# Kernel optimization log

Hardware: AMD Instinct MI355X
Metric: run time of the kernel (lower is better)

## Reference

```python
import jax, jax.numpy as jnp
import numpy as np


def _kernel_features(data, proj, is_query):
    # data: [B,S,H,D], proj: [R,D] -> features [B,S,H,R]  (FAVOR+ positive softmax kernel)
    d = data.shape[-1]
    r = proj.shape[0]
    data_normalizer = 1.0 / jnp.sqrt(jnp.sqrt(jnp.float32(d)))
    ratio = 1.0 / jnp.sqrt(jnp.float32(r))
    data_hat = jnp.einsum('bshd,rd->bshr', data_normalizer * data, proj)
    diag = (jnp.sum(data * data, axis=-1) * 0.5) * (data_normalizer * data_normalizer)
    diag = diag[..., None]  # [B,S,H,1]
    if is_query:
        m = jnp.max(data_hat, axis=-1, keepdims=True)
    else:
        m = jnp.max(data_hat)
    return ratio * (jnp.exp(data_hat - diag - m) + 1e-4)


def reference(query, key, value, Wq, bq, Wk, bk, Wv, bv, Wo, bo, proj):
    proj = jax.lax.stop_gradient(proj)
    # QKV projections: [B,S,Dm] -> [B,S,H,Dh]
    q = jnp.einsum('bsd,dhk->bshk', query, Wq) + bq
    k = jnp.einsum('bsd,dhk->bshk', key, Wk) + bk
    v = jnp.einsum('bsd,dhv->bshv', value, Wv) + bv
    q_hat = _kernel_features(q, proj, True)   # [B,S,H,R]
    k_hat = _kernel_features(k, proj, False)  # [B,S,H,R]
    # kv aggregation: 'aecr,aecd->acrd'
    kv = jnp.einsum('bshr,bshv->bhrv', k_hat, v)          # [B,H,R,Dv]
    out = jnp.einsum('bshr,bhrv->bshv', q_hat, kv)        # [B,S,H,Dv]
    # normalization: k1 = sum_s k_hat ('abcd,abc->acd'), denom = q_hat . k1
    k1 = jnp.sum(k_hat, axis=1)                           # [B,H,R]
    denom = jnp.einsum('bshr,bhr->bsh', q_hat, k1)        # [B,S,H]
    out = out / denom[..., None]
    # output projection: combine heads
    return jnp.einsum('bshv,hvd->bsd', out, Wo) + bo


def setup_inputs() -> dict:
    key0 = jax.random.key(0)
    ks = jax.random.split(key0, 10)
    B, S, Dm, H, Dh, R = 4, 4096, 1024, 16, 64, 256
    scale = 1.0 / np.sqrt(Dm)
    # Gaussian orthogonal random matrix [R, Dh], scaling=0 (chi row norms)
    blk = jax.random.normal(ks[8], (R, Dh))
    qmat, _ = jnp.linalg.qr(blk)  # R >= Dh -> q is [R, Dh]
    mult = jnp.linalg.norm(jax.random.normal(ks[9], (R, Dh)), axis=1)
    proj = mult[:, None] * qmat
    return {
        'query': jax.random.normal(ks[0], (B, S, Dm)),
        'key': jax.random.normal(ks[1], (B, S, Dm)),
        'value': jax.random.normal(ks[2], (B, S, Dm)),
        'Wq': jax.random.normal(ks[3], (Dm, H, Dh)) * scale,
        'bq': jnp.zeros((H, Dh)),
        'Wk': jax.random.normal(ks[4], (Dm, H, Dh)) * scale,
        'bk': jnp.zeros((H, Dh)),
        'Wv': jax.random.normal(ks[5], (Dm, H, Dh)) * scale,
        'bv': jnp.zeros((H, Dh)),
        'Wo': jax.random.normal(ks[6], (H, Dh, Dm)) * scale,
        'bo': jnp.zeros((Dm,)),
        'proj': proj,
    }
```

## Files before the change

kernel.cpp:

```cpp
#include <hip/hip_runtime.h>

typedef unsigned short u16;
typedef unsigned int u32;
typedef __attribute__((ext_vector_type(4))) float f32x4;
typedef __attribute__((ext_vector_type(8))) short bf16x8;

#define B_ 4
#define S_ 4096
#define H_ 16
#define DH_ 64
#define R_ 256
#define DM_ 1024
#define M_ 16384
#define ROWSTR 1024

__device__ __forceinline__ float bf2f(u16 u) {
  union { u32 i; float f; } v; v.i = ((u32)u) << 16; return v.f;
}
__device__ __forceinline__ u16 f2bf(float f) {
  union { float f; u32 i; } v; v.f = f;
  u32 x = v.i;
  return (u16)((x + 0x7FFFu + ((x >> 16) & 1u)) >> 16);
}
__device__ __forceinline__ void lds_load16(const void* g, void* l) {
  __builtin_amdgcn_global_load_lds((__attribute__((address_space(1))) void*)(g),
                                   (__attribute__((address_space(3))) void*)(l), 16, 0, 0);
}
__device__ __forceinline__ int vt_idx(int dv, int s) {
  return dv * 64 + (s ^ (dv & 0x38));
}

__global__ __launch_bounds__(256) void dtype_probe_k(const u16* __restrict__ q,
                                                     int* __restrict__ flag) {
  __shared__ int cnt_s;
  int tid = threadIdx.x;
  if (tid == 0) cnt_s = 0;
  __syncthreads();
  int c = 0;
  for (int i = tid; i < 1024; i += 256) {
    u32 e = ((u32)q[i] >> 7) & 0xFF;
    c += (e >= 134) ? 1 : 0;
  }
  atomicAdd(&cnt_s, c);
  __syncthreads();
  if (tid == 0) flag[0] = (cnt_s > 32) ? 1 : 0;
}

template <int WLO>
__global__ __launch_bounds__(256) void split_k(const void* __restrict__ src,
                                               u16* __restrict__ hi, u16* __restrict__ lo,
                                               const int* __restrict__ flag) {
  const bool f32m = flag[0] != 0;
  size_t i = ((size_t)blockIdx.x * 256 + threadIdx.x) * 8;
  if (f32m) {
    f32x4 a = *(const f32x4*)((const float*)src + i);
    f32x4 b = *(const f32x4*)((const float*)src + i + 4);
    bf16x8 h, l;
    for (int e = 0; e < 4; ++e) {
      u16 ha = f2bf(a[e]); h[e] = (short)ha; l[e] = (short)f2bf(a[e] - bf2f(ha));
      u16 hb = f2bf(b[e]); h[4 + e] = (short)hb; l[4 + e] = (short)f2bf(b[e] - bf2f(hb));
    }
    *(bf16x8*)(hi + i) = h;
    if (WLO) *(bf16x8*)(lo + i) = l;
  } else {
    bf16x8 h = *(const bf16x8*)((const u16*)src + i);
    *(bf16x8*)(hi + i) = h;
    if (WLO) {
      bf16x8 z = {0, 0, 0, 0, 0, 0, 0, 0};
      *(bf16x8*)(lo + i) = z;
    }
  }
}

__global__ __launch_bounds__(256) void transpose4_k(
    const void* __restrict__ s0, const void* __restrict__ s1,
    const void* __restrict__ s2, const void* __restrict__ s3,
    u16* __restrict__ dh0, u16* __restrict__ dl0, u16* __restrict__ dh1, u16* __restrict__ dl1,
    u16* __restrict__ dh2, u16* __restrict__ dl2, u16* __restrict__ dh3, u16* __restrict__ dl3,
    const int* __restrict__ flag) {
  __shared__ float tile[32][33];
  const bool f32m = flag[0] != 0;
  int z = blockIdx.z;
  const void* src = (z == 0) ? s0 : (z == 1) ? s1 : (z == 2) ? s2 : s3;
  u16* dh = (z == 0) ? dh0 : (z == 1) ? dh1 : (z == 2) ? dh2 : dh3;
  u16* dl = (z == 0) ? dl0 : (z == 1) ? dl1 : (z == 2) ? dl2 : dl3;
  int tx = threadIdx.x, ty = threadIdx.y;
  int x0 = blockIdx.x * 32, y0 = blockIdx.y * 32;
  for (int i = ty; i < 32; i += 8) {
    size_t idx = (size_t)(y0 + i) * DM_ + x0 + tx;
    tile[i][tx] = f32m ? ((const float*)src)[idx] : bf2f(((const u16*)src)[idx]);
  }
  __syncthreads();
  for (int i = ty; i < 32; i += 8) {
    float t = tile[tx][i];
    u16 hi = f2bf(t);
    size_t o = (size_t)(x0 + i) * DM_ + y0 + tx;
    dh[o] = hi;
    dl[o] = f2bf(t - bf2f(hi));
  }
}

__global__ __launch_bounds__(256) void projcvt_k(const void* __restrict__ p,
                                                 u16* __restrict__ ph, u16* __restrict__ pl,
                                                 const int* __restrict__ flag) {
  const bool f32m = flag[0] != 0;
  int i = blockIdx.x * 256 + threadIdx.x;
  if (i < R_ * DH_) {
    float t = f32m ? ((const float*)p)[i] : bf2f(((const u16*)p)[i]);
    u16 hi = f2bf(t);
    ph[i] = hi;
    pl[i] = f2bf(t - bf2f(hi));
  }
}

template <int PREC, int OUTMODE>
__global__ __launch_bounds__(256) void gemm_k(
    const u16* __restrict__ Ah, const u16* __restrict__ Al,
    const u16* __restrict__ Bth, const u16* __restrict__ Btl,
    const void* __restrict__ bias, void* __restrict__ C, u16* __restrict__ Clo,
    const int* __restrict__ flag) {
  __shared__ __attribute__((aligned(16))) u16 Ash[128 * 32];
  __shared__ __attribute__((aligned(16))) u16 Bsh[128 * 32];
  __shared__ __attribute__((aligned(16))) u16 Asl[128 * 32];
  __shared__ __attribute__((aligned(16))) u16 Bsl[128 * 32];
  const bool f32m = flag[0] != 0;
  const int K = DM_, N = DM_;
  const int tid = threadIdx.x, wave = tid >> 6, lane = tid & 63;
  const int lr = lane & 15, qd = lane >> 4;
  const int bm = blockIdx.x, bn = blockIdx.y;
  const int m0 = (wave & 1) * 64, n0 = (wave >> 1) * 64;
  const u16* Abh = Ah + (size_t)bm * 128 * K;
  const u16* Bbh = Bth + (size_t)bn * 128 * K;
  const u16* Abl = (PREC == 3) ? Al + (size_t)bm * 128 * K : nullptr;
  const u16* Bbl = (PREC == 3) ? Btl + (size_t)bn * 128 * K : nullptr;
  f32x4 zero = {0.f, 0.f, 0.f, 0.f};
  f32x4 acc[4][4];
  for (int i = 0; i < 4; ++i) for (int j = 0; j < 4; ++j) acc[i][j] = zero;
  for (int k0 = 0; k0 < K; k0 += 32) {
    __syncthreads();
    for (int t = 0; t < 2; ++t) {
      int c = wave + t * 4;
      int row = c * 16 + (lane >> 2);
      int kc = (lane & 3) * 8;
      size_t go = (size_t)row * K + k0 + kc;
      lds_load16(Abh + go, (void*)&Ash[c * 512]);
      lds_load16(Bbh + go, (void*)&Bsh[c * 512]);
      if (PREC == 3) {
        lds_load16(Abl + go, (void*)&Asl[c * 512]);
        lds_load16(Bbl + go, (void*)&Bsl[c * 512]);
      }
    }
    __syncthreads();
    bf16x8 ah[4], bh[4];
    for (int i = 0; i < 4; ++i) ah[i] = *(const bf16x8*)&Ash[(m0 + i * 16 + lr) * 32 + qd * 8];
    for (int j = 0; j < 4; ++j) bh[j] = *(const bf16x8*)&Bsh[(n0 + j * 16 + lr) * 32 + qd * 8];
    for (int i = 0; i < 4; ++i)
      for (int j = 0; j < 4; ++j)
        acc[i][j] = __builtin_amdgcn_mfma_f32_16x16x32_bf16(ah[i], bh[j], acc[i][j], 0, 0, 0);
    if (PREC == 3) {
      bf16x8 al[4], bl[4];
      for (int i = 0; i < 4; ++i) al[i] = *(const bf16x8*)&Asl[(m0 + i * 16 + lr) * 32 + qd * 8];
      for (int j = 0; j < 4; ++j) bl[j] = *(const bf16x8*)&Bsl[(n0 + j * 16 + lr) * 32 + qd * 8];
      for (int i = 0; i < 4; ++i)
        for (int j = 0; j < 4; ++j) {
          acc[i][j] = __builtin_amdgcn_mfma_f32_16x16x32_bf16(ah[i], bl[j], acc[i][j], 0, 0, 0);
          acc[i][j] = __builtin_amdgcn_mfma_f32_16x16x32_bf16(al[i], bh[j], acc[i][j], 0, 0, 0);
        }
    }
  }
  for (int j = 0; j < 4; ++j) {
    int n = bn * 128 + n0 + j * 16 + lr;
    float bv = f32m ? ((const float*)bias)[n] : bf2f(((const u16*)bias)[n]);
    for (int i = 0; i < 4; ++i) {
      int mr = bm * 128 + m0 + i * 16 + qd * 4;
      for (int r2 = 0; r2 < 4; ++r2) {
        float x = acc[i][j][r2] + bv;
        size_t o = (size_t)(mr + r2) * N + n;
        if (OUTMODE == 0) {
          ((u16*)C)[o] = f2bf(x);
        } else if (OUTMODE == 1) {
          u16 hi = f2bf(x);
          ((u16*)C)[o] = hi;
          Clo[o] = f2bf(x - bf2f(hi));
        } else {
          if (f32m) ((float*)C)[o] = x;
          else ((u16*)C)[o] = f2bf(x);
        }
      }
    }
  }
}

__global__ __launch_bounds__(256) void feat_max_k(
    const u16* __restrict__ khi, const u16* __restrict__ klo,
    const u16* __restrict__ ph, const u16* __restrict__ pl, float* __restrict__ pm) {
  __shared__ __attribute__((aligned(16))) u16 kth[64 * 64];
  __shared__ __attribute__((aligned(16))) u16 ktl[64 * 64];
  __shared__ float red[4];
  const int tid = threadIdx.x, wave = tid >> 6, lane = tid & 63;
  const int lr = lane & 15, qd = lane >> 4;
  int bid = blockIdx.x;
  int chunk = bid & 63, bh = bid >> 6;
  int b = bh >> 4, h = bh & 15;
  size_t base = (((size_t)b * S_ + (size_t)chunk * 64) * H_ + h) * DH_;
  {
    int s = tid >> 2, dg = (tid & 3) * 16;
    size_t go = base + (size_t)s * ROWSTR + dg;
    *(bf16x8*)&kth[s * 64 + dg]     = *(const bf16x8*)(khi + go);
    *(bf16x8*)&kth[s * 64 + dg + 8] = *(const bf16x8*)(khi + go + 8);
    *(bf16x8*)&ktl[s * 64 + dg]     = *(const bf16x8*)(klo + go);
    *(bf16x8*)&ktl[s * 64 + dg + 8] = *(const bf16x8*)(klo + go + 8);
  }
  __syncthreads();
  const int r0 = wave * 64;
  f32x4 zero = {0.f, 0.f, 0.f, 0.f};
  f32x4 acc[4][4];
  for (int i = 0; i < 4; ++i) for (int j = 0; j < 4; ++j) acc[i][j] = zero;
  for (int ks = 0; ks < 2; ++ks) {
    bf16x8 ah[4], al[4], bh_[4], bl_[4];
    for (int i = 0; i < 4; ++i) {
      ah[i] = *(const bf16x8*)&kth[(i * 16 + lr) * 64 + ks * 32 + qd * 8];
      al[i] = *(const bf16x8*)&ktl[(i * 16 + lr) * 64 + ks * 32 + qd * 8];
    }
    for (int j = 0; j < 4; ++j) {
      size_t o = (size_t)(r0 + j * 16 + lr) * DH_ + ks * 32 + qd * 8;
      bh_[j] = *(const bf16x8*)(ph + o);
      bl_[j] = *(const bf16x8*)(pl + o);
    }
    for (int i = 0; i < 4; ++i)
      for (int j = 0; j < 4; ++j) {
        acc[i][j] = __builtin_amdgcn_mfma_f32_16x16x32_bf16(ah[i], bh_[j], acc[i][j], 0, 0, 0);
        acc[i][j] = __builtin_amdgcn_mfma_f32_16x16x32_bf16(al[i], bh_[j], acc[i][j], 0, 0, 0);
        acc[i][j] = __builtin_amdgcn_mfma_f32_16x16x32_bf16(ah[i], bl_[j], acc[i][j], 0, 0, 0);
      }
  }
  float mx = -3.0e38f;
  for (int i = 0; i < 4; ++i) for (int j = 0; j < 4; ++j) for (int r2 = 0; r2 < 4; ++r2)
    mx = fmaxf(mx, acc[i][j][r2]);
  for (int m2 = 1; m2 < 64; m2 <<= 1) mx = fmaxf(mx, __shfl_xor(mx, m2, 64));
  if (lane == 0) red[wave] = mx;
  __syncthreads();
  if (tid == 0)
    pm[bid] = 0.3535533905932738f * fmaxf(fmaxf(red[0], red[1]), fmaxf(red[2], red[3]));
}

__global__ __launch_bounds__(256) void reduce_max_k(const float* __restrict__ pm,
                                                    float* __restrict__ mout) {
  __shared__ float buf[256];
  int t = threadIdx.x;
  float m = -3.0e38f;
  for (int i = t; i < 4096; i += 256) m = fmaxf(m, pm[i]);
  buf[t] = m;
  __syncthreads();
  if (t < 64) {
    float v = fmaxf(fmaxf(buf[t], buf[t + 64]), fmaxf(buf[t + 128], buf[t + 192]));
    for (int m2 = 1; m2 < 64; m2 <<= 1) v = fmaxf(v, __shfl_xor(v, m2, 64));
    if (t == 0) mout[0] = v;
  }
}

__global__ __launch_bounds__(256) void kv_accum_k(
    const u16* __restrict__ khi, const u16* __restrict__ klo,
    const u16* __restrict__ vv,
    const u16* __restrict__ ph, const u16* __restrict__ pl,
    const float* __restrict__ mptr,
    float* __restrict__ pkv, float* __restrict__ pk1, int ipb) {
  __shared__ __attribute__((aligned(16))) u16 kth[64 * 64];
  __shared__ __attribute__((aligned(16))) u16 ktl[64 * 64];
  __shared__ __attribute__((aligned(16))) u16 vTh[64 * 64];
  __shared__ __attribute__((aligned(16))) u16 khatT[256 * 72];
  __shared__ float dpart[4][64];
  __shared__ float diagl[64];
  const int tid = threadIdx.x, wave = tid >> 6, lane = tid & 63;
  const int lr = lane & 15, qd = lane >> 4;
  int bid = blockIdx.x;
  int bh = bid & 63, c = bid >> 6;
  int b = bh >> 4, h = bh & 15;
  const float mglob = mptr[0];
  const float nrm = 0.3535533905932738f;
  const float ratio = 0.0625f;
  size_t base0 = (((size_t)b * S_ + (size_t)c * ipb * 64) * H_ + h) * DH_;
  f32x4 zero = {0.f, 0.f, 0.f, 0.f};
  f32x4 acc[4][4];
  for (int i = 0; i < 4; ++i) for (int j = 0; j < 4; ++j) acc[i][j] = zero;
  float k1p[4][4];
  for (int i = 0; i < 4; ++i) for (int r2 = 0; r2 < 4; ++r2) k1p[i][r2] = 0.f;
  const int r0 = wave * 64;
  bf16x8 pfa_h[2][4], pfa_l[2][4];
  for (int ks = 0; ks < 2; ++ks)
    for (int i = 0; i < 4; ++i) {
      size_t o = (size_t)(r0 + i * 16 + lr) * DH_ + ks * 32 + qd * 8;
      pfa_h[ks][i] = *(const bf16x8*)(ph + o);
      pfa_l[ks][i] = *(const bf16x8*)(pl + o);
    }
  for (int it = 0; it < ipb; ++it) {
    size_t ibase = base0 + (size_t)it * 64 * ROWSTR;
    __syncthreads();
    {
      int s = tid >> 2, dg = (tid & 3) * 16;
      size_t go = ibase + (size_t)s * ROWSTR + dg;
      *(bf16x8*)&kth[s * 64 + dg]     = *(const bf16x8*)(khi + go);
      *(bf16x8*)&kth[s * 64 + dg + 8] = *(const bf16x8*)(khi + go + 8);
      *(bf16x8*)&ktl[s * 64 + dg]     = *(const bf16x8*)(klo + go);
      *(bf16x8*)&ktl[s * 64 + dg + 8] = *(const bf16x8*)(klo + go + 8);
    }
    {
      int s = tid >> 2;
      int dv0 = (tid & 3) * 16;
      size_t go = ibase + (size_t)s * ROWSTR + dv0;
      bf16x8 h0 = *(const bf16x8*)(vv + go);
      bf16x8 h1 = *(const bf16x8*)(vv + go + 8);
      for (int e = 0; e < 8; ++e) {
        vTh[vt_idx(dv0 + e, s)] = (u16)h0[e];
        vTh[vt_idx(dv0 + 8 + e, s)] = (u16)h1[e];
      }
    }
    __syncthreads();
    {
      int s = tid & 63, qr = tid >> 6;
      bf16x8 h0 = *(const bf16x8*)&kth[s * 64 + qr * 16];
      bf16x8 h1 = *(const bf16x8*)&kth[s * 64 + qr * 16 + 8];
      bf16x8 l0 = *(const bf16x8*)&ktl[s * 64 + qr * 16];
      bf16x8 l1 = *(const bf16x8*)&ktl[s * 64 + qr * 16 + 8];
      float sum = 0.f;
      for (int e = 0; e < 8; ++e) { float f = bf2f((u16)h0[e]) + bf2f((u16)l0[e]); sum += f * f; }
      for (int e = 0; e < 8; ++e) { float f = bf2f((u16)h1[e]) + bf2f((u16)l1[e]); sum += f * f; }
      dpart[qr][s] = sum;
    }
    __syncthreads();
    if (tid < 64)
      diagl[tid] = 0.0625f * (dpart[0][tid] + dpart[1][tid] + dpart[2][tid] + dpart[3][tid]);
    f32x4 a1[4][4];
    for (int i = 0; i < 4; ++i) for (int j = 0; j < 4; ++j) a1[i][j] = zero;
    for (int ks = 0; ks < 2; ++ks) {
      bf16x8 bh_[4], bl_[4];
      for (int j = 0; j < 4; ++j) {
        bh_[j] = *(const bf16x8*)&kth[(j * 16 + lr) * 64 + ks * 32 + qd * 8];
        bl_[j] = *(const bf16x8*)&ktl[(j * 16 + lr) * 64 + ks * 32 + qd * 8];
      }
      for (int i = 0; i < 4; ++i)
        for (int j = 0; j < 4; ++j) {
          a1[i][j] = __builtin_amdgcn_mfma_f32_16x16x32_bf16(pfa_h[ks][i], bh_[j], a1[i][j], 0, 0, 0);
          a1[i][j] = __builtin_amdgcn_mfma_f32_16x16x32_bf16(pfa_l[ks][i], bh_[j], a1[i][j], 0, 0, 0);
          a1[i][j] = __builtin_amdgcn_mfma_f32_16x16x32_bf16(pfa_h[ks][i], bl_[j], a1[i][j], 0, 0, 0);
        }
    }
    __syncthreads();
    for (int i = 0; i < 4; ++i)
      for (int r2 = 0; r2 < 4; ++r2) {
        int r = r0 + i * 16 + qd * 4 + r2;
        for (int j = 0; j < 4; ++j) {
          int s = j * 16 + lr;
          float arg = fminf(nrm * a1[i][j][r2] - diagl[s] - mglob, 30.f);
          float kh = ratio * (__expf(arg) + 1e-4f);
          u16 khb = f2bf(kh);
          khatT[r * 72 + s] = khb;
          k1p[i][r2] += bf2f(khb);
        }
      }
    __syncthreads();
    for (int ks = 0; ks < 2; ++ks) {
      bf16x8 af[4], bh_[4];
      for (int i = 0; i < 4; ++i)
        af[i] = *(const bf16x8*)&khatT[(r0 + i * 16 + lr) * 72 + ks * 32 + qd * 8];
      for (int j = 0; j < 4; ++j) {
        int dv = j * 16 + lr;
        bh_[j] = *(const bf16x8*)&vTh[vt_idx(dv, ks * 32 + qd * 8)];
      }
      for (int i = 0; i < 4; ++i)
        for (int j = 0; j < 4; ++j)
          acc[i][j] = __builtin_amdgcn_mfma_f32_16x16x32_bf16(af[i], bh_[j], acc[i][j], 0, 0, 0);
    }
  }
  size_t obase = ((size_t)c * 64 + bh) * R_;
  for (int i = 0; i < 4; ++i)
    for (int j = 0; j < 4; ++j)
      for (int r2 = 0; r2 < 4; ++r2) {
        int r = r0 + i * 16 + qd * 4 + r2;
        int dv = j * 16 + lr;
        pkv[(obase + r) * DH_ + dv] = acc[i][j][r2];
      }
  for (int i = 0; i < 4; ++i)
    for (int r2 = 0; r2 < 4; ++r2) {
      float v = k1p[i][r2];
      v += __shfl_xor(v, 1, 64); v += __shfl_xor(v, 2, 64);
      v += __shfl_xor(v, 4, 64); v += __shfl_xor(v, 8, 64);
      if (lr == 0) pk1[obase + r0 + i * 16 + qd * 4 + r2] = v;
    }
}

__global__ __launch_bounds__(256) void kv_reduce_k(
    const float* __restrict__ pkv, const float* __restrict__ pk1,
    u16* __restrict__ kvTh, u16* __restrict__ kvTl, float* __restrict__ k1, int nchunk) {
  __shared__ float tile[64][65];
  int bh = blockIdx.x, tl = blockIdx.y, t = threadIdx.x;
  if (tl == 0) {
    float s = 0.f;
    for (int c = 0; c < nchunk; ++c) s += pk1[((size_t)c * 64 + bh) * R_ + t];
    k1[(size_t)bh * R_ + t] = s;
  }
  for (int e = 0; e < 16; ++e) {
    int idx = e * 256 + t;
    int rl = idx >> 6, dv = idx & 63;
    float s = 0.f;
    for (int c = 0; c < nchunk; ++c)
      s += pkv[(((size_t)c * 64 + bh) * R_ + tl * 64 + rl) * DH_ + dv];
    tile[rl][dv] = s;
  }
  __syncthreads();
  for (int e = 0; e < 16; ++e) {
    int idx = e * 256 + t;
    int dv = idx >> 6, rl = idx & 63;
    float s = tile[rl][dv];
    u16 hi = f2bf(s);
    size_t o = ((size_t)bh * DH_ + dv) * R_ + tl * 64 + rl;
    kvTh[o] = hi;
    kvTl[o] = f2bf(s - bf2f(hi));
  }
}

__global__ __launch_bounds__(256) void q_out_k(
    const u16* __restrict__ qhi, const u16* __restrict__ qlo,
    const u16* __restrict__ ph, const u16* __restrict__ pl,
    const u16* __restrict__ kvTh, const u16* __restrict__ kvTl,
    const float* __restrict__ k1, u16* __restrict__ op) {
  __shared__ __attribute__((aligned(16))) u16 qth[64 * 64];
  __shared__ __attribute__((aligned(16))) u16 qtl[64 * 64];
  __shared__ __attribute__((aligned(16))) u16 qh[64 * 264];
  __shared__ float wrm[4][64];
  __shared__ float dpart[4][64];
  __shared__ float diagl[64];
  __shared__ float dinv[64];
  const int tid = threadIdx.x, wave = tid >> 6, lane = tid & 63;
  const int lr = lane & 15, qd = lane >> 4;
  int bid = blockIdx.x;
  int chunk = bid & 63, bh = bid >> 6;
  int b = bh >> 4, h = bh & 15;
  const float nrm = 0.3535533905932738f;
  const float ratio = 0.0625f;
  size_t base = (((size_t)b * S_ + (size_t)chunk * 64) * H_ + h) * DH_;
  const u16* kvThb = kvTh + (size_t)bh * DH_ * R_;
  const u16* kvTlb = kvTl + (size_t)bh * DH_ * R_;
  const float* k1b = k1 + (size_t)bh * R_;
  {
    int s = tid >> 2, dg = (tid & 3) * 16;
    size_t go = base + (size_t)s * ROWSTR + dg;
    *(bf16x8*)&qth[s * 64 + dg]     = *(const bf16x8*)(qhi + go);
    *(bf16x8*)&qth[s * 64 + dg + 8] = *(const bf16x8*)(qhi + go + 8);
    *(bf16x8*)&qtl[s * 64 + dg]     = *(const bf16x8*)(qlo + go);
    *(bf16x8*)&qtl[s * 64 + dg + 8] = *(const bf16x8*)(qlo + go + 8);
  }
  __syncthreads();
  {
    int s = tid & 63, qr = tid >> 6;
    bf16x8 h0 = *(const bf16x8*)&qth[s * 64 + qr * 16];
    bf16x8 h1 = *(const bf16x8*)&qth[s * 64 + qr * 16 + 8];
    bf16x8 l0 = *(const bf16x8*)&qtl[s * 64 + qr * 16];
    bf16x8 l1 = *(const bf16x8*)&qtl[s * 64 + qr * 16 + 8];
    float sum = 0.f;
    for (int e = 0; e < 8; ++e) { float f = bf2f((u16)h0[e]) + bf2f((u16)l0[e]); sum += f * f; }
    for (int e = 0; e < 8; ++e) { float f = bf2f((u16)h1[e]) + bf2f((u16)l1[e]); sum += f * f; }
    dpart[qr][s] = sum;
  }
  __syncthreads();
  if (tid < 64)
    diagl[tid] = 0.0625f * (dpart[0][tid] + dpart[1][tid] + dpart[2][tid] + dpart[3][tid]);
  f32x4 zero = {0.f, 0.f, 0.f, 0.f};
  f32x4 a1[4][4];
  for (int i = 0; i < 4; ++i) for (int j = 0; j < 4; ++j) a1[i][j] = zero;
  const int r0 = wave * 64;
  for (int ks = 0; ks < 2; ++ks) {
    bf16x8 ah[4], al[4], bh_[4], bl_[4];
    for (int i = 0; i < 4; ++i) {
      ah[i] = *(const bf16x8*)&qth[(i * 16 + lr) * 64 + ks * 32 + qd * 8];
      al[i] = *(const bf16x8*)&qtl[(i * 16 + lr) * 64 + ks * 32 + qd * 8];
    }
    for (int j = 0; j < 4; ++j) {
      size_t o = (size_t)(r0 + j * 16 + lr) * DH_ + ks * 32 + qd * 8;
      bh_[j] = *(const bf16x8*)(ph + o);
      bl_[j] = *(const bf16x8*)(pl + o);
    }
    for (int i = 0; i < 4; ++i)
      for (int j = 0; j < 4; ++j) {
        a1[i][j] = __builtin_amdgcn_mfma_f32_16x16x32_bf16(ah[i], bh_[j], a1[i][j], 0, 0, 0);
        a1[i][j] = __builtin_amdgcn_mfma_f32_16x16x32_bf16(al[i], bh_[j], a1[i][j], 0, 0, 0);
        a1[i][j] = __builtin_amdgcn_mfma_f32_16x16x32_bf16(ah[i], bl_[j], a1[i][j], 0, 0, 0);
      }
  }
  for (int i = 0; i < 4; ++i)
    for (int r2 = 0; r2 < 4; ++r2) {
      float v = fmaxf(fmaxf(a1[i][0][r2], a1[i][1][r2]), fmaxf(a1[i][2][r2], a1[i][3][r2]));
      v = fmaxf(v, __shfl_xor(v, 1, 64)); v = fmaxf(v, __shfl_xor(v, 2, 64));
      v = fmaxf(v, __shfl_xor(v, 4, 64)); v = fmaxf(v, __shfl_xor(v, 8, 64));
      if (lr == 0) wrm[wave][i * 16 + qd * 4 + r2] = v;
    }
  __syncthreads();
  for (int i = 0; i < 4; ++i)
    for (int r2 = 0; r2 < 4; ++r2) {
      int s = i * 16 + qd * 4 + r2;
      float rmax = fmaxf(fmaxf(wrm[0][s], wrm[1][s]), fmaxf(wrm[2][s], wrm[3][s]));
      float dg = diagl[s];
      for (int j = 0; j < 4; ++j) {
        float arg = fminf(nrm * (a1[i][j][r2] - rmax) - dg, 30.f);
        float qv = ratio * (__expf(arg) + 1e-4f);
        qh[s * 264 + r0 + j * 16 + lr] = f2bf(qv);
      }
    }
  __syncthreads();
  {
    float sum = 0.f;
    int s = lane;
    for (int rr = 0; rr < 8; ++rr) {
      bf16x8 v = *(const bf16x8*)&qh[s * 264 + wave * 64 + rr * 8];
      for (int e = 0; e < 8; ++e) sum += bf2f((u16)v[e]) * k1b[wave * 64 + rr * 8 + e];
    }
    dpart[wave][s] = sum;
  }
  __syncthreads();
  if (tid < 64) {
    float dn = dpart[0][tid] + dpart[1][tid] + dpart[2][tid] + dpart[3][tid];
    dinv[tid] = 1.0f / fmaxf(dn, 1e-35f);
  }
  __syncthreads();
  f32x4 a2[2][2];
  for (int i = 0; i < 2; ++i) for (int j = 0; j < 2; ++j) a2[i][j] = zero;
  const int sw = (wave & 1) * 32, dw = (wave >> 1) * 32;
  for (int ks = 0; ks < 8; ++ks) {
    bf16x8 af[2], bh_[2], bl_[2];
    for (int i = 0; i < 2; ++i)
      af[i] = *(const bf16x8*)&qh[(sw + i * 16 + lr) * 264 + ks * 32 + qd * 8];
    for (int j = 0; j < 2; ++j) {
      size_t o = (size_t)(dw + j * 16 + lr) * R_ + ks * 32 + qd * 8;
      bh_[j] = *(const bf16x8*)(kvThb + o);
      bl_[j] = *(const bf16x8*)(kvTlb + o);
    }
    for (int i = 0; i < 2; ++i)
      for (int j = 0; j < 2; ++j) {
        a2[i][j] = __builtin_amdgcn_mfma_f32_16x16x32_bf16(af[i], bh_[j], a2[i][j], 0, 0, 0);
        a2[i][j] = __builtin_amdgcn_mfma_f32_16x16x32_bf16(af[i], bl_[j], a2[i][j], 0, 0, 0);
      }
  }
  for (int i = 0; i < 2; ++i)
    for (int r2 = 0; r2 < 4; ++r2) {
      int s = sw + i * 16 + qd * 4 + r2;
      float di = dinv[s];
      for (int j = 0; j < 2; ++j) {
        int dv = dw + j * 16 + lr;
        op[base + (size_t)s * ROWSTR + dv] = f2bf(a2[i][j][r2] * di);
      }
    }
}

extern "C" void kernel_launch(void* const* d_in, const int* in_sizes, int n_in,
                              void* d_out, int out_size, void* d_ws, size_t ws_size,
                              hipStream_t stream) {
  const void* query = d_in[0];
  const void* key   = d_in[1];
  const void* value = d_in[2];
  const void* Wq = d_in[3];
  const void* bq = d_in[4];
  const void* Wk = d_in[5];
  const void* bk = d_in[6];
  const void* Wv = d_in[7];
  const void* bv = d_in[8];
  const void* Wo = d_in[9];
  const void* bo = d_in[10];
  const void* proj = d_in[11];

  char* w = (char*)d_ws;
  const size_t MB = 1024 * 1024;
  u16* WqT_h = (u16*)(w + 0 * MB);
  u16* WqT_l = (u16*)(w + 2 * MB);
  u16* WkT_h = (u16*)(w + 4 * MB);
  u16* WkT_l = (u16*)(w + 6 * MB);
  u16* WvT_h = (u16*)(w + 8 * MB);
  u16* WvT_l = (u16*)(w + 10 * MB);
  u16* WoT_h = (u16*)(w + 12 * MB);
  u16* WoT_l = (u16*)(w + 14 * MB);
  u16* kq_hi = (u16*)(w + 16 * MB);
  u16* kq_lo = (u16*)(w + 48 * MB);
  u16* vop   = (u16*)(w + 80 * MB);
  float* pk1 = (float*)(w + 112 * MB);
  u16* kvTh  = (u16*)(w + 112 * MB + 512 * 1024);
  u16* kvTl  = (u16*)(w + 114 * MB + 512 * 1024);
  float* k1  = (float*)(w + 116 * MB + 512 * 1024);
  float* pm  = (float*)(w + 116 * MB + 640 * 1024);
  float* mg  = (float*)(w + 116 * MB + 700 * 1024);
  u16* p_hi  = (u16*)(w + 116 * MB + 768 * 1024);
  u16* p_lo  = (u16*)(w + 116 * MB + 832 * 1024);
  int* flag  = (int*)(w + 116 * MB + 900 * 1024);
  float* pkv  = (float*)(w + 117 * MB);
  u16* inA_hi = (u16*)(w + 117 * MB);
  u16* inA_lo = (u16*)(w + 149 * MB);
  int nchunk = 4;
  int ipb = 64 / nchunk;

  dtype_probe_k<<<1, 256, 0, stream>>>((const u16*)query, flag);
  transpose4_k<<<dim3(32, 32, 4), dim3(32, 8), 0, stream>>>(
      Wq, Wk, Wv, Wo, WqT_h, WqT_l, WkT_h, WkT_l, WvT_h, WvT_l, WoT_h, WoT_l, flag);
  projcvt_k<<<64, 256, 0, stream>>>(proj, p_hi, p_lo, flag);
  split_k<1><<<8192, 256, 0, stream>>>(key, inA_hi, inA_lo, flag);
  gemm_k<3, 1><<<dim3(128, 8), 256, 0, stream>>>(inA_hi, inA_lo, WkT_h, WkT_l, bk, kq_hi, kq_lo, flag);
  split_k<0><<<8192, 256, 0, stream>>>(value, inA_hi, nullptr, flag);
  gemm_k<1, 0><<<dim3(128, 8), 256, 0, stream>>>(inA_hi, nullptr, WvT_h, nullptr, bv, vop, nullptr, flag);
  feat_max_k<<<4096, 256, 0, stream>>>(kq_hi, kq_lo, p_hi, p_lo, pm);
  reduce_max_k<<<1, 256, 0, stream>>>(pm, mg);
  kv_accum_k<<<nchunk * 64, 256, 0, stream>>>(kq_hi, kq_lo, vop, p_hi, p_lo, mg, pkv, pk1, ipb);
  kv_reduce_k<<<dim3(64, 4), 256, 0, stream>>>(pkv, pk1, kvTh, kvTl, k1, nchunk);
  split_k<1><<<8192, 256, 0, stream>>>(query, inA_hi, inA_lo, flag);
  gemm_k<3, 1><<<dim3(128, 8), 256, 0, stream>>>(inA_hi, inA_lo, WqT_h, WqT_l, bq, kq_hi, kq_lo, flag);
  q_out_k<<<4096, 256, 0, stream>>>(kq_hi, kq_lo, p_hi, p_lo, kvTh, kvTl, k1, vop);
  gemm_k<1, 2><<<dim3(128, 8), 256, 0, stream>>>(vop, nullptr, WoT_h, nullptr, bo, d_out, nullptr, flag);
}
```

Measured before the change: 916.0 us.

## Use direct-to-LDS swizzled loads, alias LDS buffers, fuse denom, raise chunking

Result: no change. 901.2 us (-1.6%).

```diff
diff --git a/kernel.cpp b/kernel.cpp
--- a/kernel.cpp
+++ b/kernel.cpp
@@ -203,24 +203,26 @@
   int chunk = bid & 63, bh = bid >> 6;
   int b = bh >> 4, h = bh & 15;
   size_t base = (((size_t)b * S_ + (size_t)chunk * 64) * H_ + h) * DH_;
-  {
-    int s = tid >> 2, dg = (tid & 3) * 16;
-    size_t go = base + (size_t)s * ROWSTR + dg;
-    *(bf16x8*)&kth[s * 64 + dg]     = *(const bf16x8*)(khi + go);
-    *(bf16x8*)&kth[s * 64 + dg + 8] = *(const bf16x8*)(khi + go + 8);
-    *(bf16x8*)&ktl[s * 64 + dg]     = *(const bf16x8*)(klo + go);
-    *(bf16x8*)&ktl[s * 64 + dg + 8] = *(const bf16x8*)(klo + go + 8);
+  for (int t = 0; t < 2; ++t) {
+    int cc = wave + t * 4;
+    int rr = cc * 8 + (lane >> 3);
+    int csw = (((lane & 7) ^ (rr & 7)) << 3);
+    size_t go = base + (size_t)rr * ROWSTR + csw;
+    lds_load16(khi + go, (void*)&kth[cc * 512]);
+    lds_load16(klo + go, (void*)&ktl[cc * 512]);
   }
   __syncthreads();
   const int r0 = wave * 64;
   f32x4 zero = {0.f, 0.f, 0.f, 0.f};
   f32x4 acc[4][4];
   for (int i = 0; i < 4; ++i) for (int j = 0; j < 4; ++j) acc[i][j] = zero;
+  __builtin_amdgcn_s_setprio(1);
   for (int ks = 0; ks < 2; ++ks) {
     bf16x8 ah[4], al[4], bh_[4], bl_[4];
     for (int i = 0; i < 4; ++i) {
-      ah[i] = *(const bf16x8*)&kth[(i * 16 + lr) * 64 + ks * 32 + qd * 8];
-      al[i] = *(const bf16x8*)&ktl[(i * 16 + lr) * 64 + ks * 32 + qd * 8];
+      int cof = (ks * 32 + qd * 8) ^ ((lr & 7) << 3);
+      ah[i] = *(const bf16x8*)&kth[(i * 16 + lr) * 64 + cof];
+      al[i] = *(const bf16x8*)&ktl[(i * 16 + lr) * 64 + cof];
     }
     for (int j = 0; j < 4; ++j) {
       size_t o = (size_t)(r0 + j * 16 + lr) * DH_ + ks * 32 + qd * 8;
@@ -234,6 +236,7 @@
         acc[i][j] = __builtin_amdgcn_mfma_f32_16x16x32_bf16(ah[i], bl_[j], acc[i][j], 0, 0, 0);
       }
   }
+  __builtin_amdgcn_s_setprio(0);
   float mx = -3.0e38f;
   for (int i = 0; i < 4; ++i) for (int j = 0; j < 4; ++j) for (int r2 = 0; r2 < 4; ++r2)
     mx = fmaxf(mx, acc[i][j][r2]);
@@ -265,12 +268,13 @@
     const u16* __restrict__ ph, const u16* __restrict__ pl,
     const float* __restrict__ mptr,
     float* __restrict__ pkv, float* __restrict__ pk1, int ipb) {
-  __shared__ __attribute__((aligned(16))) u16 kth[64 * 64];
-  __shared__ __attribute__((aligned(16))) u16 ktl[64 * 64];
+  __shared__ __attribute__((aligned(16))) u16 pool[256 * 72];
   __shared__ __attribute__((aligned(16))) u16 vTh[64 * 64];
-  __shared__ __attribute__((aligned(16))) u16 khatT[256 * 72];
   __shared__ float dpart[4][64];
   __shared__ float diagl[64];
+  u16* kth = pool;
+  u16* ktl = pool + 4096;
+  u16* khatT = pool;
   const int tid = threadIdx.x, wave = tid >> 6, lane = tid & 63;
   const int lr = lane & 15, qd = lane >> 4;
   int bid = blockIdx.x;
@@ -296,13 +300,13 @@
   for (int it = 0; it < ipb; ++it) {
     size_t ibase = base0 + (size_t)it * 64 * ROWSTR;
     __syncthreads();
-    {
-      int s = tid >> 2, dg = (tid & 3) * 16;
-      size_t go = ibase + (size_t)s * ROWSTR + dg;
-      *(bf16x8*)&kth[s * 64 + dg]     = *(const bf16x8*)(khi + go);
-      *(bf16x8*)&kth[s * 64 + dg + 8] = *(const bf16x8*)(khi + go + 8);
-      *(bf16x8*)&ktl[s * 64 + dg]     = *(const bf16x8*)(klo + go);
-      *(bf16x8*)&ktl[s * 64 + dg + 8] = *(const bf16x8*)(klo + go + 8);
+    for (int t = 0; t < 2; ++t) {
+      int cc = wave + t * 4;
+      int rr = cc * 8 + (lane >> 3);
+      int csw = (((lane & 7) ^ (rr & 7)) << 3);
+      size_t go = ibase + (size_t)rr * ROWSTR + csw;
+      lds_load16(khi + go, (void*)&kth[cc * 512]);
+      lds_load16(klo + go, (void*)&ktl[cc * 512]);
     }
     {
       int s = tid >> 2;
@@ -318,10 +322,11 @@
     __syncthreads();
     {
       int s = tid & 63, qr = tid >> 6;
-      bf16x8 h0 = *(const bf16x8*)&kth[s * 64 + qr * 16];
-      bf16x8 h1 = *(const bf16x8*)&kth[s * 64 + qr * 16 + 8];
-      bf16x8 l0 = *(const bf16x8*)&ktl[s * 64 + qr * 16];
-      bf16x8 l1 = *(const bf16x8*)&ktl[s * 64 + qr * 16 + 8];
+      int swz = (s & 7) << 3;
+      bf16x8 h0 = *(const bf16x8*)&kth[s * 64 + ((qr * 16) ^ swz)];
+      bf16x8 h1 = *(const bf16x8*)&kth[s * 64 + ((qr * 16 + 8) ^ swz)];
+      bf16x8 l0 = *(const bf16x8*)&ktl[s * 64 + ((qr * 16) ^ swz)];
+      bf16x8 l1 = *(const bf16x8*)&ktl[s * 64 + ((qr * 16 + 8) ^ swz)];
       float sum = 0.f;
       for (int e = 0; e < 8; ++e) { float f = bf2f((u16)h0[e]) + bf2f((u16)l0[e]); sum += f * f; }
       for (int e = 0; e < 8; ++e) { float f = bf2f((u16)h1[e]) + bf2f((u16)l1[e]); sum += f * f; }
@@ -332,11 +337,13 @@
       diagl[tid] = 0.0625f * (dpart[0][tid] + dpart[1][tid] + dpart[2][tid] + dpart[3][tid]);
     f32x4 a1[4][4];
     for (int i = 0; i < 4; ++i) for (int j = 0; j < 4; ++j) a1[i][j] = zero;
+    __builtin_amdgcn_s_setprio(1);
     for (int ks = 0; ks < 2; ++ks) {
       bf16x8 bh_[4], bl_[4];
       for (int j = 0; j < 4; ++j) {
-        bh_[j] = *(const bf16x8*)&kth[(j * 16 + lr) * 64 + ks * 32 + qd * 8];
-        bl_[j] = *(const bf16x8*)&ktl[(j * 16 + lr) * 64 + ks * 32 + qd * 8];
+        int cof = (ks * 32 + qd * 8) ^ ((lr & 7) << 3);
+        bh_[j] = *(const bf16x8*)&kth[(j * 16 + lr) * 64 + cof];
+        bl_[j] = *(const bf16x8*)&ktl[(j * 16 + lr) * 64 + cof];
       }
       for (int i = 0; i < 4; ++i)
         for (int j = 0; j < 4; ++j) {
@@ -345,6 +352,7 @@
           a1[i][j] = __builtin_amdgcn_mfma_f32_16x16x32_bf16(pfa_h[ks][i], bl_[j], a1[i][j], 0, 0, 0);
         }
     }
+    __builtin_amdgcn_s_setprio(0);
     __syncthreads();
     for (int i = 0; i < 4; ++i)
       for (int r2 = 0; r2 < 4; ++r2) {
@@ -359,6 +367,7 @@
         }
       }
     __syncthreads();
+    __builtin_amdgcn_s_setprio(1);
     for (int ks = 0; ks < 2; ++ks) {
       bf16x8 af[4], bh_[4];
       for (int i = 0; i < 4; ++i)
@@ -371,6 +380,7 @@
         for (int j = 0; j < 4; ++j)
           acc[i][j] = __builtin_amdgcn_mfma_f32_16x16x32_bf16(af[i], bh_[j], acc[i][j], 0, 0, 0);
     }
+    __builtin_amdgcn_s_setprio(0);
   }
   size_t obase = ((size_t)c * 64 + bh) * R_;
   for (int i = 0; i < 4; ++i)
@@ -419,18 +429,19 @@
   }
 }
 
-__global__ __launch_bounds__(256) void q_out_k(
+__global__ __launch_bounds__(256, 4) void q_out_k(
     const u16* __restrict__ qhi, const u16* __restrict__ qlo,
     const u16* __restrict__ ph, const u16* __restrict__ pl,
     const u16* __restrict__ kvTh, const u16* __restrict__ kvTl,
     const float* __restrict__ k1, u16* __restrict__ op) {
-  __shared__ __attribute__((aligned(16))) u16 qth[64 * 64];
-  __shared__ __attribute__((aligned(16))) u16 qtl[64 * 64];
-  __shared__ __attribute__((aligned(16))) u16 qh[64 * 264];
+  __shared__ __attribute__((aligned(16))) u16 pool[64 * 264];
   __shared__ float wrm[4][64];
   __shared__ float dpart[4][64];
   __shared__ float diagl[64];
   __shared__ float dinv[64];
+  u16* qth = pool;
+  u16* qtl = pool + 4096;
+  u16* qh = pool;
   const int tid = threadIdx.x, wave = tid >> 6, lane = tid & 63;
   const int lr = lane & 15, qd = lane >> 4;
   int bid = blockIdx.x;
@@ -442,21 +453,22 @@
   const u16* kvThb = kvTh + (size_t)bh * DH_ * R_;
   const u16* kvTlb = kvTl + (size_t)bh * DH_ * R_;
   const float* k1b = k1 + (size_t)bh * R_;
-  {
-    int s = tid >> 2, dg = (tid & 3) * 16;
-    size_t go = base + (size_t)s * ROWSTR + dg;
-    *(bf16x8*)&qth[s * 64 + dg]     = *(const bf16x8*)(qhi + go);
-    *(bf16x8*)&qth[s * 64 + dg + 8] = *(const bf16x8*)(qhi + go + 8);
-    *(bf16x8*)&qtl[s * 64 + dg]     = *(const bf16x8*)(qlo + go);
-    *(bf16x8*)&qtl[s * 64 + dg + 8] = *(const bf16x8*)(qlo + go + 8);
+  for (int t = 0; t < 2; ++t) {
+    int cc = wave + t * 4;
+    int rr = cc * 8 + (lane >> 3);
+    int csw = (((lane & 7) ^ (rr & 7)) << 3);
+    size_t go = base + (size_t)rr * ROWSTR + csw;
+    lds_load16(qhi + go, (void*)&qth[cc * 512]);
+    lds_load16(qlo + go, (void*)&qtl[cc * 512]);
   }
   __syncthreads();
   {
     int s = tid & 63, qr = tid >> 6;
-    bf16x8 h0 = *(const bf16x8*)&qth[s * 64 + qr * 16];
-    bf16x8 h1 = *(const bf16x8*)&qth[s * 64 + qr * 16 + 8];
-    bf16x8 l0 = *(const bf16x8*)&qtl[s * 64 + qr * 16];
-    bf16x8 l1 = *(const bf16x8*)&qtl[s * 64 + qr * 16 + 8];
+    int swz = (s & 7) << 3;
+    bf16x8 h0 = *(const bf16x8*)&qth[s * 64 + ((qr * 16) ^ swz)];
+    bf16x8 h1 = *(const bf16x8*)&qth[s * 64 + ((qr * 16 + 8) ^ swz)];
+    bf16x8 l0 = *(const bf16x8*)&qtl[s * 64 + ((qr * 16) ^ swz)];
+    bf16x8 l1 = *(const bf16x8*)&qtl[s * 64 + ((qr * 16 + 8) ^ swz)];
     float sum = 0.f;
     for (int e = 0; e < 8; ++e) { float f = bf2f((u16)h0[e]) + bf2f((u16)l0[e]); sum += f * f; }
     for (int e = 0; e < 8; ++e) { float f = bf2f((u16)h1[e]) + bf2f((u16)l1[e]); sum += f * f; }
@@ -469,11 +481,13 @@
   f32x4 a1[4][4];
   for (int i = 0; i < 4; ++i) for (int j = 0; j < 4; ++j) a1[i][j] = zero;
   const int r0 = wave * 64;
+  __builtin_amdgcn_s_setprio(1);
   for (int ks = 0; ks < 2; ++ks) {
     bf16x8 ah[4], al[4], bh_[4], bl_[4];
     for (int i = 0; i < 4; ++i) {
-      ah[i] = *(const bf16x8*)&qth[(i * 16 + lr) * 64 + ks * 32 + qd * 8];
-      al[i] = *(const bf16x8*)&qtl[(i * 16 + lr) * 64 + ks * 32 + qd * 8];
+      int cof = (ks * 32 + qd * 8) ^ ((lr & 7) << 3);
+      ah[i] = *(const bf16x8*)&qth[(i * 16 + lr) * 64 + cof];
+      al[i] = *(const bf16x8*)&qtl[(i * 16 + lr) * 64 + cof];
     }
     for (int j = 0; j < 4; ++j) {
       size_t o = (size_t)(r0 + j * 16 + lr) * DH_ + ks * 32 + qd * 8;
@@ -487,6 +501,7 @@
         a1[i][j] = __builtin_amdgcn_mfma_f32_16x16x32_bf16(ah[i], bl_[j], a1[i][j], 0, 0, 0);
       }
   }
+  __builtin_amdgcn_s_setprio(0);
   for (int i = 0; i < 4; ++i)
     for (int r2 = 0; r2 < 4; ++r2) {
       float v = fmaxf(fmaxf(a1[i][0][r2], a1[i][1][r2]), fmaxf(a1[i][2][r2], a1[i][3][r2]));
@@ -495,27 +510,27 @@
       if (lr == 0) wrm[wave][i * 16 + qd * 4 + r2] = v;
     }
   __syncthreads();
+  float k1v[4];
+  for (int j = 0; j < 4; ++j) k1v[j] = k1b[r0 + j * 16 + lr];
   for (int i = 0; i < 4; ++i)
     for (int r2 = 0; r2 < 4; ++r2) {
       int s = i * 16 + qd * 4 + r2;
       float rmax = fmaxf(fmaxf(wrm[0][s], wrm[1][s]), fmaxf(wrm[2][s], wrm[3][s]));
       float dg = diagl[s];
+      float dsum = 0.f;
       for (int j = 0; j < 4; ++j) {
         float arg = fminf(nrm * (a1[i][j][r2] - rmax) - dg, 30.f);
         float qv = ratio * (__expf(arg) + 1e-4f);
-        qh[s * 264 + r0 + j * 16 + lr] = f2bf(qv);
-      }
-    }
-  __syncthreads();
-  {
-    float sum = 0.f;
-    int s = lane;
-    for (int rr = 0; rr < 8; ++rr) {
-      bf16x8 v = *(const bf16x8*)&qh[s * 264 + wave * 64 + rr * 8];
-      for (int e = 0; e < 8; ++e) sum += bf2f((u16)v[e]) * k1b[wave * 64 + rr * 8 + e];
-    }
-    dpart[wave][s] = sum;
-  }
+        u16 qvb = f2bf(qv);
+        qh[s * 264 + r0 + j * 16 + lr] = qvb;
+        dsum += bf2f(qvb) * k1v[j];
+      }
+      dsum += __shfl_xor(dsum, 1, 64);
+      dsum += __shfl_xor(dsum, 2, 64);
+      dsum += __shfl_xor(dsum, 4, 64);
+      dsum += __shfl_xor(dsum, 8, 64);
+      if (lr == 0) dpart[wave][s] = dsum;
+    }
   __syncthreads();
   if (tid < 64) {
     float dn = dpart[0][tid] + dpart[1][tid] + dpart[2][tid] + dpart[3][tid];
@@ -524,11 +539,12 @@
   __syncthreads();
   f32x4 a2[2][2];
   for (int i = 0; i < 2; ++i) for (int j = 0; j < 2; ++j) a2[i][j] = zero;
-  const int sw = (wave & 1) * 32, dw = (wave >> 1) * 32;
+  const int sw2 = (wave & 1) * 32, dw = (wave >> 1) * 32;
+  __builtin_amdgcn_s_setprio(1);
   for (int ks = 0; ks < 8; ++ks) {
     bf16x8 af[2], bh_[2], bl_[2];
     for (int i = 0; i < 2; ++i)
-      af[i] = *(const bf16x8*)&qh[(sw + i * 16 + lr) * 264 + ks * 32 + qd * 8];
+      af[i] = *(const bf16x8*)&qh[(sw2 + i * 16 + lr) * 264 + ks * 32 + qd * 8];
     for (int j = 0; j < 2; ++j) {
       size_t o = (size_t)(dw + j * 16 + lr) * R_ + ks * 32 + qd * 8;
       bh_[j] = *(const bf16x8*)(kvThb + o);
@@ -540,9 +556,10 @@
         a2[i][j] = __builtin_amdgcn_mfma_f32_16x16x32_bf16(af[i], bl_[j], a2[i][j], 0, 0, 0);
       }
   }
+  __builtin_amdgcn_s_setprio(0);
   for (int i = 0; i < 2; ++i)
     for (int r2 = 0; r2 < 4; ++r2) {
-      int s = sw + i * 16 + qd * 4 + r2;
+      int s = sw2 + i * 16 + qd * 4 + r2;
       float di = dinv[s];
       for (int j = 0; j < 2; ++j) {
         int dv = dw + j * 16 + lr;
@@ -592,7 +609,7 @@
   float* pkv  = (float*)(w + 117 * MB);
   u16* inA_hi = (u16*)(w + 117 * MB);
   u16* inA_lo = (u16*)(w + 149 * MB);
-  int nchunk = 4;
+  int nchunk = 8;
   int ipb = 64 / nchunk;
 
   dtype_probe_k<<<1, 256, 0, stream>>>((const u16*)query, flag);
```
